# Kernel tuning notes

Measured on AMD Instinct MI355X. Metric: run time of the kernel, lower is better.

The kernel has to match this reference:

```python
import jax, jax.numpy as jnp
import numpy as np

SOC, EOS = 3, 2
NUM_HEADS = 12
LN_EPS = 1e-5


def setup_inputs() -> dict:
    key = jax.random.key(0)
    ks = jax.random.split(key, 24)
    B, S, D, N, FF, K = 8, 4096, 768, 1024, 3072, 640
    img = jax.random.normal(ks[0], (B, N, D), jnp.float32)
    hid = jax.random.normal(ks[1], (B, S, D), jnp.float32)
    seq = jax.random.randint(ks[2], (B, S), 4, 100)
    m = jax.random.uniform(ks[3], (B, S)) < 0.125
    seq = jnp.where(m, SOC, seq).at[:, 0].set(SOC)  # ensure >=1 SOC per row
    w = lambda k, a, b: jax.random.normal(k, (a, b), jnp.float32) * 0.02
    return {
        "img": img, "hid": hid, "seq": seq,
        "wq_s": w(ks[4], D, D), "wk_s": w(ks[5], D, D), "wv_s": w(ks[6], D, D), "wo_s": w(ks[7], D, D),
        "wq_c": w(ks[8], D, D), "wk_c": w(ks[9], D, D), "wv_c": w(ks[10], D, D), "wo_c": w(ks[11], D, D),
        "w_ff1": w(ks[12], D, FF), "w_ff2": w(ks[13], FF, D),
        "ln1_s": jnp.ones((D,)), "ln1_b": jnp.zeros((D,)),
        "ln2_s": jnp.ones((D,)), "ln2_b": jnp.zeros((D,)),
        "ln3_s": jnp.ones((D,)), "ln3_b": jnp.zeros((D,)),
        "cap": K,
    }


def _ln(x, s, b):
    mu = jnp.mean(x, axis=-1, keepdims=True)
    var = jnp.var(x, axis=-1, keepdims=True)
    return (x - mu) * jax.lax.rsqrt(var + LN_EPS) * s + b


def _mha(q_in, kv_in, wq, wk, wv, wo, key_mask):
    # q_in [B,Lq,D], kv_in [B,Lk,D], key_mask [B,Lk] bool or None
    B, Lq, D = q_in.shape
    H = NUM_HEADS
    dh = D // H
    q = (q_in @ wq).reshape(B, Lq, H, dh)
    k = (kv_in @ wk).reshape(B, -1, H, dh)
    v = (kv_in @ wv).reshape(B, -1, H, dh)
    scores = jnp.einsum("bqhd,bkhd->bhqk", q, k) / np.sqrt(dh).astype(q.dtype)
    if key_mask is not None:
        scores = jnp.where(key_mask[:, None, None, :], scores, jnp.asarray(-1e9, scores.dtype))
    att = jax.nn.softmax(scores, axis=-1)
    out = jnp.einsum("bhqk,bkhd->bqhd", att, v).reshape(B, Lq, D)
    return out @ wo


def _extract(data, mask, cap):
    # data [B,S,...], mask [B,S] bool -> packed+zero-padded [B,cap,...]
    pos = jnp.cumsum(mask, axis=1) - 1          # slot for each valid token
    pos = jnp.where(mask, pos, cap)             # invalid tokens -> dump slot
    def one(d, p):
        buf = jnp.zeros((cap + 1,) + d.shape[1:], d.dtype)
        return buf.at[p].set(d)[:cap]
        # note: dump slot cap is sliced away
    return jax.vmap(one)(data, pos), pos


def reference(img, hid, seq, wq_s, wk_s, wv_s, wo_s, wq_c, wk_c, wv_c, wo_c,
              w_ff1, w_ff2, ln1_s, ln1_b, ln2_s, ln2_b, ln3_s, ln3_b, cap):
    # mask: SOC tokens occurring before the first EOS
    soc = (seq == SOC) & (jnp.cumsum(seq == EOS, axis=1) == 0)  # [B,S]
    ext, pos = _extract(hid, soc, cap)                          # [B,K,D]
    counts = jnp.sum(soc, axis=1)                               # [B]
    run = jnp.arange(cap)[None, :] < counts[:, None]            # [B,K] valid slots

    # Blocks: pre-LN self-attn (key mask = run), cross-attn to img, FFN
    x = ext
    x = x + _mha(_ln(x, ln1_s, ln1_b), _ln(x, ln1_s, ln1_b), wq_s, wk_s, wv_s, wo_s, run)
    x = x + _mha(_ln(x, ln2_s, ln2_b), img, wq_c, wk_c, wv_c, wo_c, None)
    h = _ln(x, ln3_s, ln3_b)
    x = x + jax.nn.gelu(h @ w_ff1) @ w_ff2

    # masked_scatter back: each SOC position (b,s) takes x[b, pos[b,s]]
    idx = jnp.clip(pos, 0, cap - 1)
    gathered = jnp.take_along_axis(x, idx[:, :, None], axis=1)  # [B,S,D]
    hid_new = jnp.where(soc[:, :, None], gathered, hid)
    return hid_new, x
```

## Files before the change

kernel.cpp:

```cpp
#include <hip/hip_runtime.h>
#include <hip/hip_bf16.h>


#define B_    8
#define S_    4096
#define D_    768
#define N_    1024
#define FF_   3072
#define H_    12
#define DH_   64
#define KCAP  640
#define SOC_TOK 3
#define EOS_TOK 2

typedef __hip_bfloat16 bf16;
typedef unsigned short u16;
typedef __attribute__((ext_vector_type(8))) short short8;
typedef __attribute__((ext_vector_type(4))) float f32x4;

__device__ __forceinline__ u16 ftou16(float x){ union{bf16 b; u16 s;} c; c.b = __float2bfloat16(x); return c.s; }
__device__ __forceinline__ unsigned pk2(float lo, float hi){ return (unsigned)ftou16(lo) | ((unsigned)ftou16(hi)<<16); }

__device__ __forceinline__ f32x4 MFMA(short8 a, short8 b, f32x4 c){
  return __builtin_amdgcn_mfma_f32_16x16x32_bf16(a, b, c, 0, 0, 0);
}

__device__ __forceinline__ void gld16(const void* gp, void* lp){
  __builtin_amdgcn_global_load_lds(
    reinterpret_cast<const __attribute__((address_space(1))) unsigned int*>((size_t)gp),
    reinterpret_cast<__attribute__((address_space(3))) unsigned int*>((size_t)lp),
    16, 0, 0);
}

template<int N> __device__ __forceinline__ void vwait(){
  asm volatile("s_waitcnt vmcnt(%0)" :: "i"(N) : "memory");
}
__device__ __forceinline__ void wgbar(){ asm volatile("s_barrier" ::: "memory"); }

__device__ __forceinline__ int xcd_swz(){
  int id = blockIdx.x;
  return (id & 7) * ((int)gridDim.x >> 3) + (id >> 3);
}

__global__ __launch_bounds__(256) void scan_k(const int* __restrict__ seq,
                                              int* __restrict__ pos, int* __restrict__ src,
                                              int* __restrict__ counts){
  int b = blockIdx.x, tid = threadIdx.x;
  __shared__ int sd[256];
  __shared__ int carryE, carryS;
  if (tid==0){ carryE=0; carryS=0; }
  __syncthreads();
  for (int c=0; c<S_; c+=256){
    int s   = c + tid;
    int tok = seq[b*S_ + s];
    int isE = (tok==EOS_TOK) ? 1 : 0;
    int isS = (tok==SOC_TOK) ? 1 : 0;
    sd[tid]=isE; __syncthreads();
    for (int off=1; off<256; off<<=1){ int t_=(tid>=off)?sd[tid-off]:0; __syncthreads(); sd[tid]+=t_; __syncthreads(); }
    int eIncl = sd[tid];
    int eTot  = sd[255];
    int valid = (isS && (carryE + eIncl)==0) ? 1 : 0;
    __syncthreads();
    sd[tid]=valid; __syncthreads();
    for (int off=1; off<256; off<<=1){ int t_=(tid>=off)?sd[tid-off]:0; __syncthreads(); sd[tid]+=t_; __syncthreads(); }
    int vIncl = sd[tid];
    int vTot  = sd[255];
    if (valid){
      int slot = carryS + vIncl - 1;
      pos[b*S_ + s] = slot;
      if (slot < KCAP) src[b*KCAP + slot] = s;
    } else {
      pos[b*S_ + s] = -1;
    }
    __syncthreads();
    if (tid==0){ carryE += eTot; carryS += vTot; }
    __syncthreads();
  }
  if (tid==0) counts[b] = (carryS < KCAP) ? carryS : KCAP;
}

__global__ __launch_bounds__(256) void gather_k(const float* __restrict__ hid,
                                                const int* __restrict__ src,
                                                const int* __restrict__ counts,
                                                float* __restrict__ X){
  int bk = blockIdx.x; int b = bk / KCAP; int k = bk % KCAP;
  int tid = threadIdx.x;
  int cnt = counts[b];
  float* xr = X + (size_t)bk*D_;
  if (k < cnt){
    int s = src[b*KCAP + k];
    const float* hr = hid + ((size_t)b*S_ + s)*D_;
    xr[tid] = hr[tid]; xr[tid+256] = hr[tid+256]; xr[tid+512] = hr[tid+512];
  } else {
    xr[tid] = 0.f; xr[tid+256] = 0.f; xr[tid+512] = 0.f;
  }
}

struct TransArgs { const float* w[10]; u16* o[10]; };
__global__ __launch_bounds__(256) void transpose_all(TransArgs a){
  __shared__ float tile[32][33];
  int id = blockIdx.x;
  int wi, t, K, N;
  if (id < 4608){ wi = id/576; t = id%576; K = 768; N = 768; }
  else if (id < 6912){ wi = 8; t = id-4608; K = 768; N = 3072; }
  else { wi = 9; t = id-6912; K = 3072; N = 768; }
  const float* in = a.w[wi]; u16* out = a.o[wi];
  int nbx = N >> 5;
  int bx = t % nbx, by = t / nbx;
  int tx = threadIdx.x & 31, ty = threadIdx.x >> 5;
  #pragma unroll
  for (int i=0;i<4;++i)
    tile[ty + i*8][tx] = in[(size_t)(by*32 + ty + i*8)*N + bx*32 + tx];
  __syncthreads();
  #pragma unroll
  for (int i=0;i<4;++i)
    out[(size_t)(bx*32 + ty + i*8)*K + by*32 + tx] = ftou16(tile[tx][ty + i*8]);
}

__global__ __launch_bounds__(256) void ln_k(const float* __restrict__ X, u16* __restrict__ Y,
                                            const float* __restrict__ g, const float* __restrict__ bt){
  int r = blockIdx.x; int tid = threadIdx.x;
  const float* xr = X + (size_t)r*D_;
  float v0=xr[tid], v1=xr[tid+256], v2=xr[tid+512];
  float s1=v0+v1+v2, s2=v0*v0+v1*v1+v2*v2;
  for (int off=32; off; off>>=1){ s1+=__shfl_xor(s1,off); s2+=__shfl_xor(s2,off); }
  __shared__ float red[8];
  __shared__ float mu_s, rs_s;
  int w=tid>>6, ln=tid&63;
  if (ln==0){ red[w]=s1; red[4+w]=s2; }
  __syncthreads();
  if (tid==0){
    float S1=red[0]+red[1]+red[2]+red[3];
    float S2=red[4]+red[5]+red[6]+red[7];
    float mu = S1*(1.f/D_);
    float var= S2*(1.f/D_) - mu*mu;
    mu_s=mu; rs_s=rsqrtf(var + 1e-5f);
  }
  __syncthreads();
  float mu=mu_s, rs=rs_s;
  u16* yr = Y + (size_t)r*D_;
  yr[tid]     = ftou16((v0-mu)*rs*g[tid]     + bt[tid]);
  yr[tid+256] = ftou16((v1-mu)*rs*g[tid+256] + bt[tid+256]);
  yr[tid+512] = ftou16((v2-mu)*rs*g[tid+512] + bt[tid+512]);
}

template<int MODE, int BM, typename TA>
__global__ __launch_bounds__(256) void gemm_k(const TA* __restrict__ A, const u16* __restrict__ Bt,
                                              void* __restrict__ C0, void* __restrict__ C1, void* __restrict__ C2,
                                              int M, int N, int K, int Lkv){
  constexpr int MI  = (BM==128) ? 4 : 2;
  constexpr int LPS = (BM==128) ? 4 : 3;
  __shared__ __align__(16) u16 As[3][BM*32];
  __shared__ __align__(16) u16 Bs[3][128*32];
  int nbx = N >> 7;
  int wgid = xcd_swz();
  int bx = wgid % nbx, by = wgid / nbx;
  int tid = threadIdx.x;
  int w = tid>>6, l = tid&63, g = l>>4, c = l&15;
  int wr = w&1, wc = w>>1;
  f32x4 acc[MI][4] = {};
  float4 rg[4];
  const int NK = K/32;

  auto STAGEB = [&](int buf, int kt){
    #pragma unroll
    for (int p=0;p<2;++p){
      int row = w*32 + p*16 + (l>>2);
      int su  = (l&3) ^ ((row>>1)&3);
      gld16((const void*)(Bt + (size_t)(bx*128+row)*K + kt + su*8), (void*)&Bs[buf][(w*32+p*16)*32]);
    }
  };
  auto STAGEA16 = [&](int buf, int kt){
    if constexpr (BM==128){
      #pragma unroll
      for (int p=0;p<2;++p){
        int row = w*32 + p*16 + (l>>2);
        int su  = (l&3) ^ ((row>>1)&3);
        gld16((const void*)((const u16*)A + (size_t)(by*BM+row)*K + kt + su*8), (void*)&As[buf][(w*32+p*16)*32]);
      }
    } else {
      int row = w*16 + (l>>2);
      int su  = (l&3) ^ ((row>>1)&3);
      gld16((const void*)((const u16*)A + (size_t)(by*BM+row)*K + kt + su*8), (void*)&As[buf][(w*16)*32]);
    }
  };
  auto LOADREG = [&](int kt){
    const float* ap = (const float*)A + (size_t)(by*128 + (tid>>1))*K + kt + (tid&1)*16;
    rg[0]=*(const float4*)ap;     rg[1]=*(const float4*)(ap+4);
    rg[2]=*(const float4*)(ap+8); rg[3]=*(const float4*)(ap+12);
  };
  auto WRITEA = [&](int buf){
    int row = tid>>1, half = tid&1;
    uint4 w0,w1;
    w0.x=pk2(rg[0].x,rg[0].y); w0.y=pk2(rg[0].z,rg[0].w); w0.z=pk2(rg[1].x,rg[1].y); w0.w=pk2(rg[1].z,rg[1].w);
    w1.x=pk2(rg[2].x,rg[2].y); w1.y=pk2(rg[2].z,rg[2].w); w1.z=pk2(rg[3].x,rg[3].y); w1.w=pk2(rg[3].z,rg[3].w);
    int sw = (row>>1)&3;
    *(uint4*)&As[buf][row*32 + ((half*2  )^sw)*8] = w0;
    *(uint4*)&As[buf][row*32 + ((half*2+1)^sw)*8] = w1;
  };
  auto COMPUTE = [&](int buf){
    short8 af[MI], bfr[4];
    #pragma unroll
    for (int mi=0;mi<MI;++mi){ int row = wr*(MI*16) + mi*16 + c; af[mi]  = *(const short8*)&As[buf][row*32 + (g^((row>>1)&3))*8]; }
    #pragma unroll
    for (int ni=0;ni<4;++ni){ int row = wc*64 + ni*16 + c;       bfr[ni] = *(const short8*)&Bs[buf][row*32 + (g^((row>>1)&3))*8]; }
    #pragma unroll
    for (int mi=0;mi<MI;++mi)
      #pragma unroll
      for (int ni=0;ni<4;++ni) acc[mi][ni] = MFMA(af[mi], bfr[ni], acc[mi][ni]);
  };

  if constexpr (sizeof(TA)==4){
    LOADREG(0); STAGEB(0,0); WRITEA(0);
    __syncthreads();
    int buf = 0;
    for (int t=0;t<NK;++t){
      int ktn = (t+1)*32;
      if (t+1<NK){ LOADREG(ktn); STAGEB(buf^1, ktn); }
      COMPUTE(buf);
      if (t+1<NK) WRITEA(buf^1);
      __syncthreads();
      buf ^= 1;
    }
  } else {
    STAGEA16(0,0);  STAGEB(0,0);
    STAGEA16(1,32); STAGEB(1,32);
    vwait<LPS>();
    wgbar();
    int buf = 0;
    for (int t=0;t<NK;++t){
      if (t+2 < NK){
        int nb = buf+2; if (nb>=3) nb-=3;
        STAGEA16(nb,(t+2)*32); STAGEB(nb,(t+2)*32);
      }
      COMPUTE(buf);
      if (t < NK-2) vwait<LPS>(); else vwait<0>();
      wgbar();
      ++buf; if (buf==3) buf=0;
    }
  }

  int row0 = by*BM + wr*(MI*16), col0 = bx*128 + wc*64;
  #pragma unroll
  for (int mi=0;mi<MI;++mi)
    #pragma unroll
    for (int ni=0;ni<4;++ni)
      #pragma unroll
      for (int r=0;r<4;++r){
        int row = row0 + mi*16 + g*4 + r;
        int col = col0 + ni*16 + c;
        float v = acc[mi][ni][r];
        if (MODE==0){
          ((u16*)C0)[(size_t)row*N + col] = ftou16(v);
        } else if (MODE==1){
          ((float*)C0)[(size_t)row*N + col] += v;
        } else if (MODE==2){
          float z2 = 1.5957691216057308f*(v + 0.044715f*v*v*v);
          float e  = __expf(z2);
          float th = 1.f - 2.f/(e + 1.f);
          ((u16*)C0)[(size_t)row*N + col] = ftou16(0.5f*v*(1.f+th));
        } else if (MODE==4){
          if (col < 768)       ((u16*)C0)[(size_t)row*768 + col]       = ftou16(v);
          else if (col < 1536) ((u16*)C1)[(size_t)row*768 + col - 768] = ftou16(v);
          else {
            int vv = col - 1536; int bb = row / KCAP; int key = row - bb*KCAP;
            ((u16*)C2)[((size_t)(bb*768 + vv))*KCAP + key] = ftou16(v);
          }
        } else {
          if (col < 768) ((u16*)C0)[(size_t)row*768 + col] = ftou16(v);
          else {
            int vv = col - 768; int bb = row >> 10; int key = row & 1023;
            ((u16*)C2)[((size_t)(bb*768 + vv))*1024 + key] = ftou16(v);
          }
        }
      }
}

template<int MASKED>
__global__ __launch_bounds__(256) void attn_k(const u16* __restrict__ Q, const u16* __restrict__ Kb,
                                              const u16* __restrict__ Vt, u16* __restrict__ O,
                                              const int* __restrict__ counts, int Lk){
  __shared__ __align__(16) u16 Ks[3][64*64];
  __shared__ __align__(16) u16 Vs[3][64*64];
  __shared__ __align__(16) u16 P[4][16][72];
  int tid = threadIdx.x;
  int w = tid>>6, l = tid&63, g = l>>4, c = l&15;
  int wgid = xcd_swz();
  int qc = wgid % 5;
  int bh = wgid / 5;
  int h = bh % H_, b = bh / H_;
  int q0 = qc*128 + w*32;
  int cnt = MASKED ? counts[b] : Lk;
  int nt = (cnt + 63) >> 6;

  short8 qf[2][2];
  #pragma unroll
  for (int mi=0;mi<2;++mi){
    const u16* Qrow = Q + ((size_t)(b*KCAP + q0 + mi*16 + c))*D_ + h*DH_;
    qf[mi][0] = *(const short8*)(Qrow + g*8);
    qf[mi][1] = *(const short8*)(Qrow + 32 + g*8);
  }

  int srow8 = (l>>3);
  int sunit = l&7;
  auto STAGE = [&](int buf, int kb){
    #pragma unroll
    for (int p=0;p<2;++p){
      int r0 = w*16 + p*8;
      int rowK = r0 + srow8;
      int su = sunit ^ (rowK&7);
      gld16((const void*)(Kb + ((size_t)(b*Lk + kb + rowK))*D_ + h*DH_ + su*8), (void*)&Ks[buf][r0*64]);
      gld16((const void*)(Vt + ((size_t)(b*D_ + h*DH_ + rowK))*Lk + kb + su*8), (void*)&Vs[buf][r0*64]);
    }
  };

  f32x4 o[2][4] = {};
  float m_[2][4], l_[2][4] = {};
  #pragma unroll
  for (int mi=0;mi<2;++mi)
    #pragma unroll
    for (int r=0;r<4;++r) m_[mi][r] = -1e30f;

  STAGE(0, 0);
  if (nt > 1){ STAGE(1, 64); vwait<4>(); } else { vwait<0>(); }
  wgbar();
  int buf = 0;
  for (int t=0; t<nt; ++t){
    int kb = t*64;
    if (t+2 < nt){
      int nb = buf+2; if (nb>=3) nb-=3;
      STAGE(nb, kb+128);
    }
    short8 fr[4][2];
    #pragma unroll
    for (int nb=0;nb<4;++nb)
      #pragma unroll
      for (int kh=0;kh<2;++kh)
        fr[nb][kh] = *(const short8*)&Ks[buf][(nb*16+c)*64 + (((kh<<2)|g) ^ (c&7))*8];
    f32x4 z[2][4];
    #pragma unroll
    for (int mi=0;mi<2;++mi)
      #pragma unroll
      for (int nb=0;nb<4;++nb){
        f32x4 zz = {0.f,0.f,0.f,0.f};
        zz = MFMA(qf[mi][0], fr[nb][0], zz);
        zz = MFMA(qf[mi][1], fr[nb][1], zz);
        z[mi][nb] = zz;
      }
    float pv[2][4][4];
    #pragma unroll
    for (int nb=0;nb<4;++nb){
      bool msk = MASKED && (kb + nb*16 + c >= cnt);
      #pragma unroll
      for (int mi=0;mi<2;++mi)
        #pragma unroll
        for (int r=0;r<4;++r) pv[mi][nb][r] = msk ? -1e30f : z[mi][nb][r]*0.125f;
    }
    float scl[2][4];
    #pragma unroll
    for (int mi=0;mi<2;++mi){
      #pragma unroll
      for (int r=0;r<4;++r){
        float v = fmaxf(fmaxf(pv[mi][0][r],pv[mi][1][r]), fmaxf(pv[mi][2][r],pv[mi][3][r]));
        v = fmaxf(v, __shfl_xor(v,1)); v = fmaxf(v, __shfl_xor(v,2));
        v = fmaxf(v, __shfl_xor(v,4)); v = fmaxf(v, __shfl_xor(v,8));
        float nm = fmaxf(m_[mi][r], v);
        scl[mi][r] = __expf(m_[mi][r] - nm);
        m_[mi][r] = nm;
      }
      #pragma unroll
      for (int r=0;r<4;++r){
        float acc2 = 0.f;
        #pragma unroll
        for (int nb=0;nb<4;++nb){
          float e = __expf(pv[mi][nb][r] - m_[mi][r]);
          pv[mi][nb][r] = e; acc2 += e;
        }
        acc2 += __shfl_xor(acc2,1); acc2 += __shfl_xor(acc2,2);
        acc2 += __shfl_xor(acc2,4); acc2 += __shfl_xor(acc2,8);
        l_[mi][r] = l_[mi][r]*scl[mi][r] + acc2;
      }
      #pragma unroll
      for (int nbd=0;nbd<4;++nbd)
        #pragma unroll
        for (int r=0;r<4;++r) o[mi][nbd][r] *= scl[mi][r];
    }
    #pragma unroll
    for (int nbd=0;nbd<4;++nbd)
      #pragma unroll
      for (int kh=0;kh<2;++kh)
        fr[nbd][kh] = *(const short8*)&Vs[buf][(nbd*16+c)*64 + (((kh<<2)|g) ^ (c&7))*8];
    #pragma unroll
    for (int mi=0;mi<2;++mi){
      #pragma unroll
      for (int nb=0;nb<4;++nb)
        #pragma unroll
        for (int r=0;r<4;++r) P[w][g*4+r][nb*16+c] = ftou16(pv[mi][nb][r]);
      short8 pa0 = *(const short8*)&P[w][c][g*8];
      short8 pa1 = *(const short8*)&P[w][c][32 + g*8];
      #pragma unroll
      for (int nbd=0;nbd<4;++nbd){
        o[mi][nbd] = MFMA(pa0, fr[nbd][0], o[mi][nbd]);
        o[mi][nbd] = MFMA(pa1, fr[nbd][1], o[mi][nbd]);
      }
    }
    if (t < nt-2) vwait<4>(); else vwait<0>();
    wgbar();
    ++buf; if (buf==3) buf=0;
  }
  #pragma unroll
  for (int mi=0;mi<2;++mi)
    #pragma unroll
    for (int nbd=0;nbd<4;++nbd)
      #pragma unroll
      for (int r=0;r<4;++r)
        O[((size_t)(b*KCAP + q0 + mi*16 + g*4 + r))*D_ + h*DH_ + nbd*16 + c] = ftou16(o[mi][nbd][r] / l_[mi][r]);
}

__global__ __launch_bounds__(256) void scatter_k(const int* __restrict__ pos, const float* __restrict__ X,
                                                 const float* __restrict__ hid, float* __restrict__ out0){
  int bs = blockIdx.x; int tid = threadIdx.x;
  int b = bs >> 12;
  int p = pos[bs];
  float* orow = out0 + (size_t)bs*D_;
  if (p >= 0){
    int pc = p < KCAP ? p : (KCAP-1);
    const float* xr = X + ((size_t)(b*KCAP + pc))*D_;
    orow[tid]     = xr[tid];
    orow[tid+256] = xr[tid+256];
    orow[tid+512] = xr[tid+512];
  } else {
    const float* hr = hid + (size_t)bs*D_;
    orow[tid]     = hr[tid];
    orow[tid+256] = hr[tid+256];
    orow[tid+512] = hr[tid+512];
  }
}

__global__ __launch_bounds__(256) void xout_k(const float* __restrict__ X, float* __restrict__ out1){
  int i = blockIdx.x*256 + threadIdx.x;
  out1[i] = X[i];
}

extern "C" void kernel_launch(void* const* d_in, const int* in_sizes, int n_in,
                              void* d_out, int out_size, void* d_ws, size_t ws_size,
                              hipStream_t stream){
  const float* img  = (const float*)d_in[0];
  const float* hid  = (const float*)d_in[1];
  const int*   seq  = (const int*)  d_in[2];
  const float* W[10] = { (const float*)d_in[3], (const float*)d_in[4], (const float*)d_in[5], (const float*)d_in[6],
                         (const float*)d_in[7], (const float*)d_in[8], (const float*)d_in[9], (const float*)d_in[10],
                         (const float*)d_in[11], (const float*)d_in[12] };
  const float* ln1s = (const float*)d_in[13];
  const float* ln1b = (const float*)d_in[14];
  const float* ln2s = (const float*)d_in[15];
  const float* ln2b = (const float*)d_in[16];
  const float* ln3s = (const float*)d_in[17];
  const float* ln3b = (const float*)d_in[18];

  char* ws = (char*)d_ws;
  int*   pos    = (int*)  (ws + 0);
  int*   src    = (int*)  (ws + 131072);
  int*   counts = (int*)  (ws + 151552);
  float* X      = (float*)(ws + 151808);
  u16*   T0     = (u16*)  (ws + 15880448);
  u16*   Qb     = (u16*)  (ws + 23744768);
  u16*   Kb     = (u16*)  (ws + 31609088);
  u16*   Vt     = (u16*)  (ws + 44192000);
  u16*   AO     = (u16*)  (ws + 56774912);
  u16*   Wt     = (u16*)  (ws + 64639232);
  u16*   MID    = Qb;

  u16* wqkv_st = Wt + 0ull*589824;
  u16* wo_st   = Wt + 3ull*589824;
  u16* wq_ct   = Wt + 4ull*589824;
  u16* wkv_ct  = Wt + 5ull*589824;
  u16* wo_ct   = Wt + 7ull*589824;
  u16* wff1t   = Wt + 8ull*589824;
  u16* wff2t   = wff1t + 2359296;

  float* out0 = (float*)d_out;
  float* out1 = out0 + (size_t)B_*S_*D_;

  const int MKD = B_*KCAP;

  TransArgs ta;
  for (int i=0;i<10;++i) ta.w[i] = W[i];
  for (int i=0;i<8;++i)  ta.o[i] = Wt + (size_t)i*589824;
  ta.o[8] = wff1t; ta.o[9] = wff2t;
  transpose_all<<<9216, 256, 0, stream>>>(ta);

  scan_k  <<<B_,      256, 0, stream>>>(seq, pos, src, counts);
  gather_k<<<B_*KCAP, 256, 0, stream>>>(hid, src, counts, X);

  const int G_QKV = (MKD/128)*(2304/128);
  const int G_N768= (MKD/64)*(768/128);
  const int G_KV  = ((B_*N_)/128)*(1536/128);
  const int G_FF1 = (MKD/128)*(FF_/128);
  const int G_ATT = B_*H_*5;

  ln_k<<<MKD, 256, 0, stream>>>(X, T0, ln1s, ln1b);
  gemm_k<4,128,u16><<<G_QKV, 256, 0, stream>>>(T0, wqkv_st, Qb, Kb, Vt, MKD, 2304, D_, KCAP);
  attn_k<1><<<G_ATT, 256, 0, stream>>>(Qb, Kb, Vt, AO, counts, KCAP);
  gemm_k<1,64,u16><<<G_N768, 256, 0, stream>>>(AO, wo_st, X, nullptr, nullptr, MKD, D_, D_, 0);

  ln_k<<<MKD, 256, 0, stream>>>(X, T0, ln2s, ln2b);
  gemm_k<0,64,u16>   <<<G_N768, 256, 0, stream>>>(T0,  wq_ct,  Qb, nullptr, nullptr, MKD,   D_,   D_, 0);
  gemm_k<5,128,float><<<G_KV,   256, 0, stream>>>(img, wkv_ct, Kb, nullptr, Vt,      B_*N_, 1536, D_, N_);
  attn_k<0><<<G_ATT, 256, 0, stream>>>(Qb, Kb, Vt, AO, counts, N_);
  gemm_k<1,64,u16><<<G_N768, 256, 0, stream>>>(AO, wo_ct, X, nullptr, nullptr, MKD, D_, D_, 0);

  ln_k<<<MKD, 256, 0, stream>>>(X, T0, ln3s, ln3b);
  gemm_k<2,128,u16><<<G_FF1,  256, 0, stream>>>(T0,  wff1t, MID, nullptr, nullptr, MKD, FF_, D_,  0);
  gemm_k<1,64,u16> <<<G_N768, 256, 0, stream>>>(MID, wff2t, X,   nullptr, nullptr, MKD, D_,  FF_, 0);

  scatter_k<<<B_*S_, 256, 0, stream>>>(pos, X, hid, out0);
  xout_k  <<<(MKD*D_)/256, 256, 0, stream>>>(X, out1);
}
```

Baseline: 478.4 us.

## Fuse small kernels and merge independent cross-attention GEMMs into one launch

```diff
diff --git a/kernel.cpp b/kernel.cpp
--- a/kernel.cpp
+++ b/kernel.cpp
@@ -42,10 +42,9 @@
   return (id & 7) * ((int)gridDim.x >> 3) + (id >> 3);
 }
 
-__global__ __launch_bounds__(256) void scan_k(const int* __restrict__ seq,
-                                              int* __restrict__ pos, int* __restrict__ src,
-                                              int* __restrict__ counts){
-  int b = blockIdx.x, tid = threadIdx.x;
+__device__ void scan_body(const int* __restrict__ seq, int* __restrict__ pos,
+                          int* __restrict__ src, int* __restrict__ counts, int b){
+  int tid = threadIdx.x;
   __shared__ int sd[256];
   __shared__ int carryE, carryS;
   if (tid==0){ carryE=0; carryS=0; }
@@ -79,27 +78,13 @@
   if (tid==0) counts[b] = (carryS < KCAP) ? carryS : KCAP;
 }
 
-__global__ __launch_bounds__(256) void gather_k(const float* __restrict__ hid,
-                                                const int* __restrict__ src,
-                                                const int* __restrict__ counts,
-                                                float* __restrict__ X){
-  int bk = blockIdx.x; int b = bk / KCAP; int k = bk % KCAP;
-  int tid = threadIdx.x;
-  int cnt = counts[b];
-  float* xr = X + (size_t)bk*D_;
-  if (k < cnt){
-    int s = src[b*KCAP + k];
-    const float* hr = hid + ((size_t)b*S_ + s)*D_;
-    xr[tid] = hr[tid]; xr[tid+256] = hr[tid+256]; xr[tid+512] = hr[tid+512];
-  } else {
-    xr[tid] = 0.f; xr[tid+256] = 0.f; xr[tid+512] = 0.f;
-  }
-}
-
 struct TransArgs { const float* w[10]; u16* o[10]; };
-__global__ __launch_bounds__(256) void transpose_all(TransArgs a){
+__global__ __launch_bounds__(256) void transpose_scan_k(TransArgs a, const int* __restrict__ seq,
+                                                        int* __restrict__ pos, int* __restrict__ src,
+                                                        int* __restrict__ counts){
+  int id = blockIdx.x;
+  if (id >= 9216){ scan_body(seq, pos, src, counts, id - 9216); return; }
   __shared__ float tile[32][33];
-  int id = blockIdx.x;
   int wi, t, K, N;
   if (id < 4608){ wi = id/576; t = id%576; K = 768; N = 768; }
   else if (id < 6912){ wi = 8; t = id-4608; K = 768; N = 3072; }
@@ -115,6 +100,42 @@
   #pragma unroll
   for (int i=0;i<4;++i)
     out[(size_t)(bx*32 + ty + i*8)*K + by*32 + tx] = ftou16(tile[tx][ty + i*8]);
+}
+
+__global__ __launch_bounds__(256) void gather_ln_k(const float* __restrict__ hid,
+                                                   const int* __restrict__ src,
+                                                   const int* __restrict__ counts,
+                                                   const float* __restrict__ g, const float* __restrict__ bt,
+                                                   float* __restrict__ X, u16* __restrict__ T0){
+  int bk = blockIdx.x; int b = bk / KCAP; int k = bk % KCAP;
+  int tid = threadIdx.x;
+  float v0, v1, v2;
+  if (k < counts[b]){
+    const float* hr = hid + ((size_t)b*S_ + src[b*KCAP + k])*D_;
+    v0 = hr[tid]; v1 = hr[tid+256]; v2 = hr[tid+512];
+  } else { v0 = v1 = v2 = 0.f; }
+  float* xr = X + (size_t)bk*D_;
+  xr[tid] = v0; xr[tid+256] = v1; xr[tid+512] = v2;
+  float s1=v0+v1+v2, s2=v0*v0+v1*v1+v2*v2;
+  for (int off=32; off; off>>=1){ s1+=__shfl_xor(s1,off); s2+=__shfl_xor(s2,off); }
+  __shared__ float red[8];
+  __shared__ float mu_s, rs_s;
+  int w=tid>>6, ln=tid&63;
+  if (ln==0){ red[w]=s1; red[4+w]=s2; }
+  __syncthreads();
+  if (tid==0){
+    float S1=red[0]+red[1]+red[2]+red[3];
+    float S2=red[4]+red[5]+red[6]+red[7];
+    float mu = S1*(1.f/D_);
+    float var= S2*(1.f/D_) - mu*mu;
+    mu_s=mu; rs_s=rsqrtf(var + 1e-5f);
+  }
+  __syncthreads();
+  float mu=mu_s, rs=rs_s;
+  u16* yr = T0 + (size_t)bk*D_;
+  yr[tid]     = ftou16((v0-mu)*rs*g[tid]     + bt[tid]);
+  yr[tid+256] = ftou16((v1-mu)*rs*g[tid+256] + bt[tid+256]);
+  yr[tid+512] = ftou16((v2-mu)*rs*g[tid+512] + bt[tid+512]);
 }
 
 __global__ __launch_bounds__(256) void ln_k(const float* __restrict__ X, u16* __restrict__ Y,
@@ -144,22 +165,21 @@
   yr[tid+512] = ftou16((v2-mu)*rs*g[tid+512] + bt[tid+512]);
 }
 
-template<int MODE, int BM, typename TA>
-__global__ __launch_bounds__(256) void gemm_k(const TA* __restrict__ A, const u16* __restrict__ Bt,
-                                              void* __restrict__ C0, void* __restrict__ C1, void* __restrict__ C2,
-                                              int M, int N, int K, int Lkv){
-  constexpr int MI  = (BM==128) ? 4 : 2;
-  constexpr int LPS = (BM==128) ? 4 : 3;
-  __shared__ __align__(16) u16 As[3][BM*32];
-  __shared__ __align__(16) u16 Bs[3][128*32];
+template<int MODE, typename TA>
+__device__ __forceinline__ void gemm_body(char* ldsp, const TA* __restrict__ A, const u16* __restrict__ Bt,
+                                          void* __restrict__ C0, void* __restrict__ C1, void* __restrict__ C2,
+                                          int wgid, int N, int K){
+  constexpr int BM = 64, MI = 2, LPS = 3;
+  constexpr int NBUF = (sizeof(TA)==4) ? 2 : 3;
+  u16* As = (u16*)ldsp;
+  u16* Bs = (u16*)(ldsp + NBUF*(BM*32)*2);
   int nbx = N >> 7;
-  int wgid = xcd_swz();
   int bx = wgid % nbx, by = wgid / nbx;
   int tid = threadIdx.x;
   int w = tid>>6, l = tid&63, g = l>>4, c = l&15;
   int wr = w&1, wc = w>>1;
   f32x4 acc[MI][4] = {};
-  float4 rg[4];
+  float4 rg0, rg1;
   const int NK = K/32;
 
   auto STAGEB = [&](int buf, int kt){
@@ -167,43 +187,31 @@
     for (int p=0;p<2;++p){
       int row = w*32 + p*16 + (l>>2);
       int su  = (l&3) ^ ((row>>1)&3);
-      gld16((const void*)(Bt + (size_t)(bx*128+row)*K + kt + su*8), (void*)&Bs[buf][(w*32+p*16)*32]);
+      gld16((const void*)(Bt + (size_t)(bx*128+row)*K + kt + su*8), (void*)&Bs[buf*128*32 + (w*32+p*16)*32]);
     }
   };
   auto STAGEA16 = [&](int buf, int kt){
-    if constexpr (BM==128){
-      #pragma unroll
-      for (int p=0;p<2;++p){
-        int row = w*32 + p*16 + (l>>2);
-        int su  = (l&3) ^ ((row>>1)&3);
-        gld16((const void*)((const u16*)A + (size_t)(by*BM+row)*K + kt + su*8), (void*)&As[buf][(w*32+p*16)*32]);
-      }
-    } else {
-      int row = w*16 + (l>>2);
-      int su  = (l&3) ^ ((row>>1)&3);
-      gld16((const void*)((const u16*)A + (size_t)(by*BM+row)*K + kt + su*8), (void*)&As[buf][(w*16)*32]);
-    }
+    int row = w*16 + (l>>2);
+    int su  = (l&3) ^ ((row>>1)&3);
+    gld16((const void*)((const u16*)A + (size_t)(by*BM+row)*K + kt + su*8), (void*)&As[buf*BM*32 + (w*16)*32]);
   };
   auto LOADREG = [&](int kt){
-    const float* ap = (const float*)A + (size_t)(by*128 + (tid>>1))*K + kt + (tid&1)*16;
-    rg[0]=*(const float4*)ap;     rg[1]=*(const float4*)(ap+4);
-    rg[2]=*(const float4*)(ap+8); rg[3]=*(const float4*)(ap+12);
+    const float* ap = (const float*)A + (size_t)(by*BM + (tid>>2))*K + kt + (tid&3)*8;
+    rg0 = *(const float4*)ap; rg1 = *(const float4*)(ap+4);
   };
   auto WRITEA = [&](int buf){
-    int row = tid>>1, half = tid&1;
-    uint4 w0,w1;
-    w0.x=pk2(rg[0].x,rg[0].y); w0.y=pk2(rg[0].z,rg[0].w); w0.z=pk2(rg[1].x,rg[1].y); w0.w=pk2(rg[1].z,rg[1].w);
-    w1.x=pk2(rg[2].x,rg[2].y); w1.y=pk2(rg[2].z,rg[2].w); w1.z=pk2(rg[3].x,rg[3].y); w1.w=pk2(rg[3].z,rg[3].w);
+    int row = tid>>2, unit = tid&3;
+    uint4 wv;
+    wv.x=pk2(rg0.x,rg0.y); wv.y=pk2(rg0.z,rg0.w); wv.z=pk2(rg1.x,rg1.y); wv.w=pk2(rg1.z,rg1.w);
     int sw = (row>>1)&3;
-    *(uint4*)&As[buf][row*32 + ((half*2  )^sw)*8] = w0;
-    *(uint4*)&As[buf][row*32 + ((half*2+1)^sw)*8] = w1;
+    *(uint4*)&As[buf*BM*32 + row*32 + (unit^sw)*8] = wv;
   };
   auto COMPUTE = [&](int buf){
     short8 af[MI], bfr[4];
     #pragma unroll
-    for (int mi=0;mi<MI;++mi){ int row = wr*(MI*16) + mi*16 + c; af[mi]  = *(const short8*)&As[buf][row*32 + (g^((row>>1)&3))*8]; }
-    #pragma unroll
-    for (int ni=0;ni<4;++ni){ int row = wc*64 + ni*16 + c;       bfr[ni] = *(const short8*)&Bs[buf][row*32 + (g^((row>>1)&3))*8]; }
+    for (int mi=0;mi<MI;++mi){ int row = wr*32 + mi*16 + c; af[mi]  = *(const short8*)&As[buf*BM*32 + row*32 + (g^((row>>1)&3))*8]; }
+    #pragma unroll
+    for (int ni=0;ni<4;++ni){ int row = wc*64 + ni*16 + c;  bfr[ni] = *(const short8*)&Bs[buf*128*32 + row*32 + (g^((row>>1)&3))*8]; }
     #pragma unroll
     for (int mi=0;mi<MI;++mi)
       #pragma unroll
@@ -240,7 +248,7 @@
     }
   }
 
-  int row0 = by*BM + wr*(MI*16), col0 = bx*128 + wc*64;
+  int row0 = by*BM + wr*32, col0 = bx*128 + wc*64;
   #pragma unroll
   for (int mi=0;mi<MI;++mi)
     #pragma unroll
@@ -259,6 +267,11 @@
           float e  = __expf(z2);
           float th = 1.f - 2.f/(e + 1.f);
           ((u16*)C0)[(size_t)row*N + col] = ftou16(0.5f*v*(1.f+th));
+        } else if (MODE==6){
+          size_t idx = (size_t)row*N + col;
+          float fin = ((float*)C0)[idx] + v;
+          ((float*)C0)[idx] = fin;
+          ((float*)C1)[idx] = fin;
         } else if (MODE==4){
           if (col < 768)       ((u16*)C0)[(size_t)row*768 + col]       = ftou16(v);
           else if (col < 1536) ((u16*)C1)[(size_t)row*768 + col - 768] = ftou16(v);
@@ -274,6 +287,25 @@
           }
         }
       }
+}
+
+template<int MODE, typename TA>
+__global__ __launch_bounds__(256) void gemm_k(const TA* __restrict__ A, const u16* __restrict__ Bt,
+                                              void* __restrict__ C0, void* __restrict__ C1, void* __restrict__ C2,
+                                              int N, int K){
+  constexpr int LDSZ = ((sizeof(TA)==4)?2:3) * (64+128)*32*2;
+  __shared__ __align__(16) char pool[LDSZ];
+  gemm_body<MODE,TA>(pool, A, Bt, C0, C1, C2, xcd_swz(), N, K);
+}
+
+__global__ __launch_bounds__(256) void gemm_dual_k(const u16* __restrict__ T0, const u16* __restrict__ wq_ct,
+                                                   u16* __restrict__ Qb,
+                                                   const float* __restrict__ img, const u16* __restrict__ wkv_ct,
+                                                   u16* __restrict__ Kb, u16* __restrict__ Vt){
+  __shared__ __align__(16) char pool[3*(64+128)*32*2];
+  int wgid = xcd_swz();
+  if (wgid < 480) gemm_body<0,u16>  (pool, T0,  wq_ct,  Qb, nullptr, nullptr, wgid,      768,  768);
+  else            gemm_body<5,float>(pool, img, wkv_ct, Kb, nullptr, Vt,      wgid-480, 1536,  768);
 }
 
 template<int MASKED>
@@ -437,11 +469,6 @@
   }
 }
 
-__global__ __launch_bounds__(256) void xout_k(const float* __restrict__ X, float* __restrict__ out1){
-  int i = blockIdx.x*256 + threadIdx.x;
-  out1[i] = X[i];
-}
-
 extern "C" void kernel_launch(void* const* d_in, const int* in_sizes, int n_in,
                               void* d_out, int out_size, void* d_ws, size_t ws_size,
                               hipStream_t stream){
@@ -482,38 +509,32 @@
   float* out0 = (float*)d_out;
   float* out1 = out0 + (size_t)B_*S_*D_;
 
-  const int MKD = B_*KCAP;
-
   TransArgs ta;
   for (int i=0;i<10;++i) ta.w[i] = W[i];
   for (int i=0;i<8;++i)  ta.o[i] = Wt + (size_t)i*589824;
   ta.o[8] = wff1t; ta.o[9] = wff2t;
-  transpose_all<<<9216, 256, 0, stream>>>(ta);
-
-  scan_k  <<<B_,      256, 0, stream>>>(seq, pos, src, counts);
-  gather_k<<<B_*KCAP, 256, 0, stream>>>(hid, src, counts, X);
-
-  const int G_QKV = (MKD/128)*(2304/128);
-  const int G_N768= (MKD/64)*(768/128);
-  const int G_KV  = ((B_*N_)/128)*(1536/128);
-  const int G_FF1 = (MKD/128)*(FF_/128);
-  const int G_ATT = B_*H_*5;
-
-  ln_k<<<MKD, 256, 0, stream>>>(X, T0, ln1s, ln1b);
-  gemm_k<4,128,u16><<<G_QKV, 256, 0, stream>>>(T0, wqkv_st, Qb, Kb, Vt, MKD, 2304, D_, KCAP);
+
+  transpose_scan_k<<<9224, 256, 0, stream>>>(ta, seq, pos, src, counts);
+  gather_ln_k<<<B_*KCAP, 256, 0, stream>>>(hid, src, counts, ln1s, ln1b, X, T0);
+
+  const int G_QKV  = (5120/64)*(2304/128);
+  const int G_N768 = (5120/64)*(768/128);
+  const int G_FF1  = (5120/64)*(3072/128);
+  const int G_DUAL = 480 + (8192/64)*(1536/128);
+  const int G_ATT  = B_*H_*5;
+
+  gemm_k<4,u16><<<G_QKV, 256, 0, stream>>>(T0, wqkv_st, Qb, Kb, Vt, 2304, 768);
   attn_k<1><<<G_ATT, 256, 0, stream>>>(Qb, Kb, Vt, AO, counts, KCAP);
-  gemm_k<1,64,u16><<<G_N768, 256, 0, stream>>>(AO, wo_st, X, nullptr, nullptr, MKD, D_, D_, 0);
-
-  ln_k<<<MKD, 256, 0, stream>>>(X, T0, ln2s, ln2b);
-  gemm_k<0,64,u16>   <<<G_N768, 256, 0, stream>>>(T0,  wq_ct,  Qb, nullptr, nullptr, MKD,   D_,   D_, 0);
-  gemm_k<5,128,float><<<G_KV,   256, 0, stream>>>(img, wkv_ct, Kb, nullptr, Vt,      B_*N_, 1536, D_, N_);
+  gemm_k<1,u16><<<G_N768, 256, 0, stream>>>(AO, wo_st, X, nullptr, nullptr, 768, 768);
+
+  ln_k<<<5120, 256, 0, stream>>>(X, T0, ln2s, ln2b);
+  gemm_dual_k<<<G_DUAL, 256, 0, stream>>>(T0, wq_ct, Qb, img, wkv_ct, Kb, Vt);
   attn_k<0><<<G_ATT, 256, 0, stream>>>(Qb, Kb, Vt, AO, counts, N_);
-  gemm_k<1,64,u16><<<G_N768, 256, 0, stream>>>(AO, wo_ct, X, nullptr, nullptr, MKD, D_, D_, 0);
-
-  ln_k<<<MKD, 256, 0, stream>>>(X, T0, ln3s, ln3b);
-  gemm_k<2,128,u16><<<G_FF1,  256, 0, stream>>>(T0,  wff1t, MID, nullptr, nullptr, MKD, FF_, D_,  0);
-  gemm_k<1,64,u16> <<<G_N768, 256, 0, stream>>>(MID, wff2t, X,   nullptr, nullptr, MKD, D_,  FF_, 0);
+  gemm_k<1,u16><<<G_N768, 256, 0, stream>>>(AO, wo_ct, X, nullptr, nullptr, 768, 768);
+
+  ln_k<<<5120, 256, 0, stream>>>(X, T0, ln3s, ln3b);
+  gemm_k<2,u16><<<G_FF1, 256, 0, stream>>>(T0, wff1t, MID, nullptr, nullptr, 3072, 768);
+  gemm_k<6,u16><<<G_N768, 256, 0, stream>>>(MID, wff2t, X, out1, nullptr, 768, 3072);
 
   scatter_k<<<B_*S_, 256, 0, stream>>>(pos, X, hid, out0);
-  xout_k  <<<(MKD*D_)/256, 256, 0, stream>>>(X, out1);
-}
+}
```

Measured after the change: 474.4 us. No clear change (-0.8%).
